# Optimization experiments

Measured on AMD Instinct MI355X. Metric: run time of the kernel, lower is better.

Reference implementation:

```python
import jax, jax.numpy as jnp
import numpy as np

M = 4096            # neurons = orientations (model_type=3)
BATCH = 256         # batch of stimulus orientations (vmapped simulate)
TAU = 0.02
DT = 0.001
T_SIM = 0.06
ALPHA = 0.9
KAPPA = np.pi / 4.0
NUM_STEPS = int(T_SIM / DT)  # 60


def _build_ring_W(m=M, kappa=KAPPA, alpha=ALPHA):
    # Model 3: W_ring[i,j] = V(phi_i - phi_j), then scaled so max eigenvalue = alpha.
    phi = 2.0 * np.pi * np.arange(m, dtype=np.float64) / m
    diff = phi[:, None] - phi[None, :]
    W_ring = np.exp((np.cos(diff) - 1.0) / kappa ** 2)
    # W_ring is symmetric -> eigvalsh gives real spectrum; max eig = max real part.
    max_eig = np.linalg.eigvalsh(W_ring).max()
    return (W_ring * (alpha / max_eig)).astype(np.float32)


def setup_inputs() -> dict:
    key = jax.random.key(0)
    k_theta, _ = jax.random.split(key)
    theta = jax.random.uniform(k_theta, (BATCH,), dtype=jnp.float32,
                               minval=0.0, maxval=2.0 * np.pi)
    W = jnp.asarray(_build_ring_W())
    return {"theta": theta, "W": W}


def reference(theta, W):
    """Batched RNNModel.simulate for model_type=3 (B = I, so B @ h = h).
    Returns (t_record [S+1], r_record [S+1, n, batch])."""
    n = W.shape[0]
    phi = (2.0 * jnp.pi / n) * jnp.arange(n, dtype=jnp.float32)
    # h[i, b] = exp((cos(phi_i - theta_b) - 1) / kappa^2)
    h = jnp.exp((jnp.cos(phi[:, None] - theta[None, :]) - 1.0) / KAPPA ** 2)
    coef = jnp.float32(DT / TAU)
    inv_dt = jnp.float32(1.0 / DT)

    def step_fn(r, s):
        imp = jnp.where(s == 0, inv_dt, jnp.float32(0.0))  # delta input only at t=0
        r_new = r + coef * (-r + W @ r + imp * h)
        return r_new, r_new

    r0 = jnp.zeros_like(h)
    _, r_record = jax.lax.scan(step_fn, r0, jnp.arange(NUM_STEPS + 1))
    t_record = DT * jnp.arange(NUM_STEPS + 1, dtype=jnp.float32)
    return t_record, r_record
```

## Files before the change

kernel.cpp:

```cpp
#include <hip/hip_runtime.h>
#include <math.h>


#define NN      4096
#define NB      256
#define NSTEPS  61
#define KM      4
#define NJ      9

#define PHI_STEP 0.0015339807878856412f
#define INV_K2   1.6211389382774044f

typedef float fx4 __attribute__((ext_vector_type(4)));

#define L_OFF   64
#define UV_OFF  2048
#define SUV_OFF 8192

#define NROWS   (NSTEPS * NN)
#define NTRAIL  (NROWS / 16)

__device__ __forceinline__ float phiF(int i) { return PHI_STEP * (float)i; }

__global__ void __launch_bounds__(256)
rnn_ring_prep(const float* __restrict__ theta, const float* __restrict__ W,
              float* __restrict__ ws, float* __restrict__ out) {
    int tid = threadIdx.x;
    __shared__ float red[4][NJ];
    int wid = tid >> 6, lane = tid & 63;

    float c1 = cosf(phiF(tid)), s1 = sinf(phiF(tid));
    const float cR = cosf(256.0f * PHI_STEP);
    const float sR = sinf(256.0f * PHI_STEP);

    if (blockIdx.x == 256) {
        float acc[KM + 1];
#pragma unroll
        for (int k = 0; k <= KM; ++k) acc[k] = 0.0f;
#pragma unroll
        for (int it = 0; it < 16; ++it) {
            float w = W[tid + (it << 8)];
            acc[0] += w;
            acc[1] += w * c1;
            float ckm1 = 1.0f, ck = c1;
#pragma unroll
            for (int k = 2; k <= KM; ++k) {
                float cn = 2.0f * c1 * ck - ckm1;
                ckm1 = ck; ck = cn;
                acc[k] += w * cn;
            }
            float c1n = c1 * cR - s1 * sR;
            float s1n = s1 * cR + c1 * sR;
            c1 = c1n; s1 = s1n;
        }
#pragma unroll
        for (int k = 0; k <= KM; ++k) {
            float x = acc[k];
            x += __shfl_xor(x, 32); x += __shfl_xor(x, 16); x += __shfl_xor(x, 8);
            x += __shfl_xor(x, 4);  x += __shfl_xor(x, 2);  x += __shfl_xor(x, 1);
            acc[k] = x;
        }
        if (lane == 0) {
#pragma unroll
            for (int k = 0; k <= KM; ++k) red[wid][k] = acc[k];
        }
        __syncthreads();
        if (tid <= KM) {
            float wk  = red[0][tid] + red[1][tid] + red[2][tid] + red[3][tid];
            float lam = 0.95f + 0.05f * wk;
            float p = 1.0f;
            for (int s = 0; s < NSTEPS; ++s) {
                ws[L_OFF + s * (KM + 1) + tid] = p;
                p *= lam;
            }
        }
        if (tid >= 64 && tid < 64 + NSTEPS)
            out[tid - 64] = 0.001f * (float)(tid - 64);
    } else {
        int b = blockIdx.x;
        float th  = theta[b];
        float cth = cosf(th), sth = sinf(th);
        float uv[NJ];
#pragma unroll
        for (int j = 0; j < NJ; ++j) uv[j] = 0.0f;
#pragma unroll
        for (int it = 0; it < 16; ++it) {
            float cd = c1 * cth + s1 * sth;
            float hh = __expf((cd - 1.0f) * INV_K2);
            uv[0]      += hh;
            uv[1]      += hh * c1;
            uv[KM + 1] += hh * s1;
            float ckm1 = 1.0f, skm1 = 0.0f, ck = c1, sk = s1;
#pragma unroll
            for (int k = 2; k <= KM; ++k) {
                float cn = 2.0f * c1 * ck - ckm1;
                float sn = 2.0f * c1 * sk - skm1;
                ckm1 = ck; skm1 = sk; ck = cn; sk = sn;
                uv[k]      += hh * cn;
                uv[KM + k] += hh * sn;
            }
            float c1n = c1 * cR - s1 * sR;
            float s1n = s1 * cR + c1 * sR;
            c1 = c1n; s1 = s1n;
        }
#pragma unroll
        for (int j = 0; j < NJ; ++j) {
            float x = uv[j];
            x += __shfl_xor(x, 32); x += __shfl_xor(x, 16); x += __shfl_xor(x, 8);
            x += __shfl_xor(x, 4);  x += __shfl_xor(x, 2);  x += __shfl_xor(x, 1);
            uv[j] = x;
        }
        if (lane == 0) {
#pragma unroll
            for (int j = 0; j < NJ; ++j) red[wid][j] = uv[j];
        }
        __syncthreads();
        if (tid < NJ) {
            float x  = red[0][tid] + red[1][tid] + red[2][tid] + red[3][tid];
            float sc = (tid == 0) ? (50.0f / 4096.0f) : (100.0f / 4096.0f);
            x *= sc;
            ws[UV_OFF  + tid * NB + b]               = x;
            ws[SUV_OFF + tid * NB + ((b - 3) & 255)] = x;
        }
    }
}

__global__ void __launch_bounds__(256)
rnn_ring_kC(const float* __restrict__ ws, float* __restrict__ out) {
    int blk = blockIdx.x;
    int tid = threadIdx.x;

    if (blk < NSTEPS * 64) {
        int s    = blk >> 6;
        int i0   = (blk & 63) << 6;
        int lane = tid & 63;
        int w    = tid >> 6;

        float lam[KM + 1];
#pragma unroll
        for (int k = 0; k <= KM; ++k) lam[k] = ws[L_OFF + s * (KM + 1) + k];

        fx4 P[NJ];
#pragma unroll
        for (int j = 0; j < NJ; ++j) {
            fx4 v = *reinterpret_cast<const fx4*>(&ws[SUV_OFF + j * NB + 4 * lane]);
            P[j] = v * ((j <= KM) ? lam[j] : lam[j - KM]);
        }

        int row0 = i0 + 16 * w;
        float ph = phiF(row0);
        float c1 = cosf(ph), s1 = sinf(ph);
        const float cD = cosf(PHI_STEP), sD = sinf(PHI_STEP);
        float* rowptr = out + NSTEPS + ((size_t)s * NN + row0) * NB;
        float pax = 0.0f;
        bool b63 = (lane == 63);

#pragma unroll
        for (int r = 0; r < 16; ++r) {
            float t2 = 2.0f * c1;
            fx4 a = P[0] + c1 * P[1] + s1 * P[KM + 1];
            float ck = c1, sk = s1, ckm1 = 1.0f, skm1 = 0.0f;
#pragma unroll
            for (int k = 2; k <= KM; ++k) {
                float cn = t2 * ck - ckm1;
                float sn = t2 * sk - skm1;
                ckm1 = ck; ck = cn; skm1 = sk; sk = sn;
                a += cn * P[k] + sn * P[KM + k];
            }
            if (b63) {
                if (r > 0) {
                    fx4 q; q.x = pax; q.y = a.y; q.z = a.z; q.w = a.w;
                    *reinterpret_cast<fx4*>(rowptr - 1) = q;
                }
                pax = a.x;
            } else {
                *reinterpret_cast<fx4*>(rowptr + 3 + 4 * lane) = a;
            }
            float c1n = c1 * cD - s1 * sD;
            float s1n = s1 * cD + c1 * sD;
            c1 = c1n; s1 = s1n;
            rowptr += NB;
        }
    } else {
        int g = (blk - NSTEPS * 64) * 256 + tid;
        if (g < NTRAIL) {
            int rg  = 16 * g + 15;
            int s   = rg >> 12;
            int row = rg & (NN - 1);
            float ph = phiF(row);
            float c  = cosf(ph), sv = sinf(ph);
            float CN[KM + 1], SN[KM + 1];
            CN[0] = 1.0f; SN[0] = 0.0f; CN[1] = c; SN[1] = sv;
#pragma unroll
            for (int k = 2; k <= KM; ++k) {
                CN[k] = 2.0f * c * CN[k - 1] - CN[k - 2];
                SN[k] = 2.0f * c * SN[k - 1] - SN[k - 2];
            }
            float x = 0.0f;
#pragma unroll
            for (int k = 0; k <= KM; ++k) {
                float t = CN[k] * ws[UV_OFF + k * NB + 255];
                if (k >= 1) t += SN[k] * ws[UV_OFF + (KM + k) * NB + 255];
                x += ws[L_OFF + s * (KM + 1) + k] * t;
            }
            float* dst = out + NSTEPS + (size_t)rg * NB + 255;
            if (rg == NROWS - 1) {
                *dst = x;
            } else {
                int rg2  = rg + 1;
                int s2   = rg2 >> 12;
                int row2 = rg2 & (NN - 1);
                float ph2 = phiF(row2);
                float c2 = cosf(ph2), sv2 = sinf(ph2);
                float CN2[KM + 1], SN2[KM + 1];
                CN2[0] = 1.0f; SN2[0] = 0.0f; CN2[1] = c2; SN2[1] = sv2;
#pragma unroll
                for (int k = 2; k <= KM; ++k) {
                    CN2[k] = 2.0f * c2 * CN2[k - 1] - CN2[k - 2];
                    SN2[k] = 2.0f * c2 * SN2[k - 1] - SN2[k - 2];
                }
                float y = 0.0f, z = 0.0f, ww = 0.0f;
#pragma unroll
                for (int k = 0; k <= KM; ++k) {
                    float l2 = ws[L_OFF + s2 * (KM + 1) + k];
                    float t0 = CN2[k] * ws[UV_OFF + k * NB + 0];
                    float t1 = CN2[k] * ws[UV_OFF + k * NB + 1];
                    float t2 = CN2[k] * ws[UV_OFF + k * NB + 2];
                    if (k >= 1) {
                        t0 += SN2[k] * ws[UV_OFF + (KM + k) * NB + 0];
                        t1 += SN2[k] * ws[UV_OFF + (KM + k) * NB + 1];
                        t2 += SN2[k] * ws[UV_OFF + (KM + k) * NB + 2];
                    }
                    y += l2 * t0; z += l2 * t1; ww += l2 * t2;
                }
                fx4 q; q.x = x; q.y = y; q.z = z; q.w = ww;
                *reinterpret_cast<fx4*>(dst) = q;
            }
        } else if (g == NTRAIL) {
#pragma unroll
            for (int b = 0; b < 3; ++b) {
                float v = 0.0f;
#pragma unroll
                for (int k = 0; k <= KM; ++k) v += ws[UV_OFF + k * NB + b];
                out[NSTEPS + b] = v;
            }
        }
    }
}

extern "C" void kernel_launch(void* const* d_in, const int* in_sizes, int n_in,
                              void* d_out, int out_size, void* d_ws, size_t ws_size,
                              hipStream_t stream) {
    (void)in_sizes; (void)n_in; (void)out_size; (void)ws_size;
    const float* theta = (const float*)d_in[0];
    const float* W     = (const float*)d_in[1];
    float* out = (float*)d_out;
    float* ws  = (float*)d_ws;

    rnn_ring_prep<<<dim3(257),             dim3(256), 0, stream>>>(theta, W, ws, out);
    rnn_ring_kC <<<dim3(NSTEPS * 64 + 64), dim3(256), 0, stream>>>(ws, out);
}
```

Baseline: 50.24 us.

## Precompute rotated harmonic coefficients to cut per-row FLOPs and enlarge row tiles

Each wave now writes 64 rows instead of 16, in groups of four. Harmonics 3 and 4 are evaluated once per group of four. The in-group phase offsets for harmonics 1 and 2 are folded into precomputed rotated coefficient vectors. This lowers per-row ALU work and per-block setup overhead, but it uses more registers and gives a 4x smaller grid. The trailing-row fixup grid shrinks to match.

```diff
diff --git a/kernel.cpp b/kernel.cpp
--- a/kernel.cpp
+++ b/kernel.cpp
@@ -11,6 +11,17 @@
 #define PHI_STEP 0.0015339807878856412f
 #define INV_K2   1.6211389382774044f
 
+#define C1D 0.99999882345148f
+#define S1D 0.00153398018629f
+#define C2D 0.99999529380590f
+#define S2D 0.00306795676300f
+#define C3D 0.99998941106350f
+#define S3D 0.00460192612050f
+#define C4D 0.99998117522360f
+#define S4D 0.00613588464910f
+#define C6D 0.99995764455250f
+#define S6D 0.00920375478170f
+
 typedef float fx4 __attribute__((ext_vector_type(4)));
 
 #define L_OFF   64
@@ -18,7 +29,7 @@
 #define SUV_OFF 8192
 
 #define NROWS   (NSTEPS * NN)
-#define NTRAIL  (NROWS / 16)
+#define NTRAIL  (NROWS / 64)
 
 __device__ __forceinline__ float phiF(int i) { return PHI_STEP * (float)i; }
 
@@ -130,9 +141,9 @@
     int blk = blockIdx.x;
     int tid = threadIdx.x;
 
-    if (blk < NSTEPS * 64) {
-        int s    = blk >> 6;
-        int i0   = (blk & 63) << 6;
+    if (blk < NSTEPS * 16) {
+        int s    = blk >> 4;
+        int i0   = (blk & 15) << 8;
         int lane = tid & 63;
         int w    = tid >> 6;
 
@@ -140,51 +151,66 @@
 #pragma unroll
         for (int k = 0; k <= KM; ++k) lam[k] = ws[L_OFF + s * (KM + 1) + k];
 
-        fx4 P[NJ];
+        fx4 Q[NJ];
 #pragma unroll
         for (int j = 0; j < NJ; ++j) {
             fx4 v = *reinterpret_cast<const fx4*>(&ws[SUV_OFF + j * NB + 4 * lane]);
-            P[j] = v * ((j <= KM) ? lam[j] : lam[j - KM]);
-        }
-
-        int row0 = i0 + 16 * w;
+            Q[j] = v * ((j <= KM) ? lam[j] : lam[j - KM]);
+        }
+        fx4 P0 = Q[0];
+        fx4 Qc3 = Q[3], Qs3 = Q[KM + 3], Qc4 = Q[4], Qs4 = Q[KM + 4];
+
+        fx4 Pc1[4], Ps1[4], Pc2[4], Ps2[4];
+        Pc1[0] = Q[1];                      Ps1[0] = Q[KM + 1];
+        Pc2[0] = Q[2];                      Ps2[0] = Q[KM + 2];
+        Pc1[1] = C1D * Q[1] + S1D * Q[KM + 1];  Ps1[1] = C1D * Q[KM + 1] - S1D * Q[1];
+        Pc1[2] = C2D * Q[1] + S2D * Q[KM + 1];  Ps1[2] = C2D * Q[KM + 1] - S2D * Q[1];
+        Pc1[3] = C3D * Q[1] + S3D * Q[KM + 1];  Ps1[3] = C3D * Q[KM + 1] - S3D * Q[1];
+        Pc2[1] = C2D * Q[2] + S2D * Q[KM + 2];  Ps2[1] = C2D * Q[KM + 2] - S2D * Q[2];
+        Pc2[2] = C4D * Q[2] + S4D * Q[KM + 2];  Ps2[2] = C4D * Q[KM + 2] - S4D * Q[2];
+        Pc2[3] = C6D * Q[2] + S6D * Q[KM + 2];  Ps2[3] = C6D * Q[KM + 2] - S6D * Q[2];
+
+        int row0 = i0 + 64 * w;
         float ph = phiF(row0);
         float c1 = cosf(ph), s1 = sinf(ph);
-        const float cD = cosf(PHI_STEP), sD = sinf(PHI_STEP);
+        float t2 = 2.0f * c1;
+        float c2 = t2 * c1 - 1.0f, s2 = t2 * s1;
+        float c3 = t2 * c2 - c1,   s3 = t2 * s2 - s1;
+        float c4 = t2 * c3 - c2,   s4 = t2 * s3 - s2;
+
         float* rowptr = out + NSTEPS + ((size_t)s * NN + row0) * NB;
         float pax = 0.0f;
         bool b63 = (lane == 63);
 
-#pragma unroll
-        for (int r = 0; r < 16; ++r) {
-            float t2 = 2.0f * c1;
-            fx4 a = P[0] + c1 * P[1] + s1 * P[KM + 1];
-            float ck = c1, sk = s1, ckm1 = 1.0f, skm1 = 0.0f;
-#pragma unroll
-            for (int k = 2; k <= KM; ++k) {
-                float cn = t2 * ck - ckm1;
-                float sn = t2 * sk - skm1;
-                ckm1 = ck; ck = cn; skm1 = sk; sk = sn;
-                a += cn * P[k] + sn * P[KM + k];
-            }
-            if (b63) {
-                if (r > 0) {
-                    fx4 q; q.x = pax; q.y = a.y; q.z = a.z; q.w = a.w;
-                    *reinterpret_cast<fx4*>(rowptr - 1) = q;
+        for (int g = 0; g < 16; ++g) {
+            fx4 ahi = P0 + c3 * Qc3 + s3 * Qs3 + c4 * Qc4 + s4 * Qs4;
+#pragma unroll
+            for (int d = 0; d < 4; ++d) {
+                fx4 a = ahi + c1 * Pc1[d] + s1 * Ps1[d]
+                            + c2 * Pc2[d] + s2 * Ps2[d];
+                if (b63) {
+                    if ((g | d) != 0) {
+                        fx4 q; q.x = pax; q.y = a.y; q.z = a.z; q.w = a.w;
+                        *reinterpret_cast<fx4*>(rowptr - 1) = q;
+                    }
+                    pax = a.x;
+                } else {
+                    *reinterpret_cast<fx4*>(rowptr + 3 + 4 * lane) = a;
                 }
-                pax = a.x;
-            } else {
-                *reinterpret_cast<fx4*>(rowptr + 3 + 4 * lane) = a;
-            }
-            float c1n = c1 * cD - s1 * sD;
-            float s1n = s1 * cD + c1 * sD;
+                rowptr += NB;
+            }
+            float c1n = c1 * C4D - s1 * S4D;
+            float s1n = s1 * C4D + c1 * S4D;
             c1 = c1n; s1 = s1n;
-            rowptr += NB;
+            t2 = 2.0f * c1;
+            c2 = t2 * c1 - 1.0f; s2 = t2 * s1;
+            c3 = t2 * c2 - c1;   s3 = t2 * s2 - s1;
+            c4 = t2 * c3 - c2;   s4 = t2 * s3 - s2;
         }
     } else {
-        int g = (blk - NSTEPS * 64) * 256 + tid;
+        int g = (blk - NSTEPS * 16) * 256 + tid;
         if (g < NTRAIL) {
-            int rg  = 16 * g + 15;
+            int rg  = 64 * g + 63;
             int s   = rg >> 12;
             int row = rg & (NN - 1);
             float ph = phiF(row);
@@ -225,13 +251,13 @@
                     float l2 = ws[L_OFF + s2 * (KM + 1) + k];
                     float t0 = CN2[k] * ws[UV_OFF + k * NB + 0];
                     float t1 = CN2[k] * ws[UV_OFF + k * NB + 1];
-                    float t2 = CN2[k] * ws[UV_OFF + k * NB + 2];
+                    float t2v = CN2[k] * ws[UV_OFF + k * NB + 2];
                     if (k >= 1) {
-                        t0 += SN2[k] * ws[UV_OFF + (KM + k) * NB + 0];
-                        t1 += SN2[k] * ws[UV_OFF + (KM + k) * NB + 1];
-                        t2 += SN2[k] * ws[UV_OFF + (KM + k) * NB + 2];
+                        t0  += SN2[k] * ws[UV_OFF + (KM + k) * NB + 0];
+                        t1  += SN2[k] * ws[UV_OFF + (KM + k) * NB + 1];
+                        t2v += SN2[k] * ws[UV_OFF + (KM + k) * NB + 2];
                     }
-                    y += l2 * t0; z += l2 * t1; ww += l2 * t2;
+                    y += l2 * t0; z += l2 * t1; ww += l2 * t2v;
                 }
                 fx4 q; q.x = x; q.y = y; q.z = z; q.w = ww;
                 *reinterpret_cast<fx4*>(dst) = q;
@@ -258,5 +284,5 @@
     float* ws  = (float*)d_ws;
 
     rnn_ring_prep<<<dim3(257),             dim3(256), 0, stream>>>(theta, W, ws, out);
-    rnn_ring_kC <<<dim3(NSTEPS * 64 + 64), dim3(256), 0, stream>>>(ws, out);
+    rnn_ring_kC <<<dim3(NSTEPS * 16 + 16), dim3(256), 0, stream>>>(ws, out);
 }
```

New measurement: 48.55 us. -3.4%, faster.
